# Kernel tuning notes

Hardware: AMD Instinct MI355X
Metric: run time of the kernel (lower is better)

## Reference

```python
import jax, jax.numpy as jnp
import numpy as np

HEADS = 8
NUM_CLASS = 4
DIM = 512


def setup_inputs() -> dict:
    key = jax.random.key(0)
    k0, k1, k2, k3 = jax.random.split(key, 4)
    B, N, C = 4, 1280, DIM  # N = (NUM_CLASS+1) * 256 tokens per group
    x = jax.random.normal(k0, (B, N, C), jnp.float32)
    # modality-presence mask: 1 = modality available, 0 = missing
    mask = jax.random.randint(k1, (B, NUM_CLASS), 0, 2).astype(jnp.int32)
    s = 1.0 / np.sqrt(C)
    W_qkv = jax.random.normal(k2, (C, 3 * C), jnp.float32) * s  # qkv (no bias)
    W_proj = jax.random.normal(k3, (C, C), jnp.float32) * s
    b_proj = jnp.zeros((C,), jnp.float32)
    return {"x": x, "mask": mask, "W_qkv": W_qkv, "W_proj": W_proj, "b_proj": b_proj}


def reference(x, mask, W_qkv, W_proj, b_proj):
    B, N, C = x.shape
    H = HEADS
    hd = C // H
    scale = hd ** -0.5
    # qkv: [B,N,3C] -> [3,B,H,N,hd]
    qkv = (x @ W_qkv).reshape(B, N, 3, H, hd).transpose(2, 0, 3, 1, 4)
    q, k, v = qkv[0], qkv[1], qkv[2]
    attn = jnp.einsum('bhqd,bhkd->bhqk', q, k) * scale  # [B,H,N,N]
    # block mask: keys belonging to missing modality groups are disallowed;
    # the last (fusion) group is always allowed -> every row has valid keys.
    np_ = N // (NUM_CLASS + 1)  # tokens per group
    group = jnp.arange(N) // np_  # [N], group id in [0, NUM_CLASS]
    allowed = jnp.concatenate(
        [mask.astype(jnp.float32), jnp.ones((B, 1), jnp.float32)], axis=1)  # [B, NUM_CLASS+1]
    col_ok = allowed[:, group]  # [B, N] per-key allowance
    attn = jnp.where(col_ok[:, None, None, :] == 0, -jnp.inf, attn)
    attn = jax.nn.softmax(attn, axis=-1)
    out = jnp.einsum('bhqk,bhkd->bhqd', attn, v)  # [B,H,N,hd]
    out = out.transpose(0, 2, 1, 3).reshape(B, N, C)
    out = out @ W_proj + b_proj
    return out, attn
```

## Files before the change

### kernel.cpp

```cpp
#include <hip/hip_runtime.h>
#include <math.h>

#define BATCH 4
#define NSEQ  1280
#define CDIM  512
#define HEADS 8
#define HD    64
#define NT    20
#define NQT   20

typedef __attribute__((ext_vector_type(8))) short bf16x8;
typedef __attribute__((ext_vector_type(4))) float f32x4;

#define MFMA16(a,b,c) __builtin_amdgcn_mfma_f32_16x16x32_bf16(a,b,c,0,0,0)

__device__ __forceinline__ unsigned short f2bf(float f) {
    union { float f; unsigned int u; } v; v.f = f;
    unsigned int r = v.u + 0x7fffu + ((v.u >> 16) & 1u);
    return (unsigned short)(r >> 16);
}
__device__ __forceinline__ float bf2f(unsigned short h) {
    union { unsigned int u; float f; } v; v.u = ((unsigned int)h) << 16;
    return v.f;
}
__device__ __forceinline__ void gload_lds16(const void* g, void* l) {
    __builtin_amdgcn_global_load_lds(
        (const __attribute__((address_space(1))) unsigned int*)g,
        (__attribute__((address_space(3))) unsigned int*)l, 16, 0, 0);
}

__global__ __launch_bounds__(256)
void conv_kernel(const float* __restrict__ x, const float* __restrict__ Wq,
                 const float* __restrict__ Wp, unsigned short* __restrict__ xb,
                 unsigned short* __restrict__ Wqt, unsigned short* __restrict__ Wpt)
{
    __shared__ float lt[64][65];
    const int bx = blockIdx.x;
    const int tid = threadIdx.x;
    if (bx < 1280) {
        const int u = bx * 256 + tid;
        const int m = u >> 6;
        const int b6 = u & 63;
        const int chunk = b6 >> 3;
        const int blk = b6 & 7;
        const float* src = x + (size_t)m * 512 + b6 * 8;
        bf16x8 hv;
        #pragma unroll
        for (int j = 0; j < 8; ++j) hv[j] = (short)f2bf(src[j]);
        *(bf16x8*)(xb + (size_t)m * 512 + chunk * 64 + ((blk ^ (m & 7)) * 8)) = hv;
    } else {
        int wi = bx - 1280;
        const float* W; unsigned short* Wt; int N, kt, nt; bool isQ;
        if (wi < 192) { W = Wq; Wt = Wqt; N = 1536; kt = wi / 24; nt = wi % 24; isQ = true; }
        else { wi -= 192; W = Wp; Wt = Wpt; N = 512; kt = wi / 8; nt = wi % 8; isQ = false; }
        const int k0 = kt * 64, n0 = nt * 64;
        {
            const int r = tid >> 4;
            const int c = (tid & 15) * 4;
            #pragma unroll
            for (int i = 0; i < 4; ++i) {
                const float4 v = *(const float4*)(W + (size_t)(k0 + r + i * 16) * N + n0 + c);
                lt[r + i * 16][c + 0] = v.x; lt[r + i * 16][c + 1] = v.y;
                lt[r + i * 16][c + 2] = v.z; lt[r + i * 16][c + 3] = v.w;
            }
        }
        __syncthreads();
        #pragma unroll
        for (int i = 0; i < 2; ++i) {
            const int u = tid + i * 256;
            const int n = u >> 3;
            const int blk = u & 7;
            const int kin = (blk ^ (n & 7)) * 8;
            const float sc = (isQ && (n0 + n) < 512) ? 0.125f : 1.0f;
            bf16x8 o;
            #pragma unroll
            for (int j = 0; j < 8; ++j) o[j] = (short)f2bf(lt[kin + j][n] * sc);
            *(bf16x8*)(Wt + (size_t)(n0 + n) * 512 + k0 + blk * 8) = o;
        }
    }
}

template<int WM, int WN, bool BIAS, bool OUTBF16>
__global__ __launch_bounds__(256)
void gemm_bf16(const unsigned short* __restrict__ A,
               const unsigned short* __restrict__ B,
               const float* __restrict__ bias, void* __restrict__ Cv,
               int M, int N, int KA)
{
    constexpr int BM = 2 * WM, BN = 2 * WN;
    constexpr int MI = WM / 16, NI = WN / 16;
    __shared__ __align__(16) unsigned short smem[(BM + BN) * 64];
    unsigned short* As = smem;
    unsigned short* Bs = smem + BM * 64;

    const int tid = threadIdx.x;
    const int w = tid >> 6, lane = tid & 63;
    const int l15 = lane & 15, hi = lane >> 4;
    const int wr = w >> 1, wc = w & 1;
    const int m0 = blockIdx.y * BM, n0 = blockIdx.x * BN;

    f32x4 acc[MI][NI];
    #pragma unroll
    for (int mi = 0; mi < MI; ++mi)
        #pragma unroll
        for (int ni = 0; ni < NI; ++ni) acc[mi][ni] = (f32x4){0.f, 0.f, 0.f, 0.f};

    constexpr int LA = BM * 128 / 4096;
    constexpr int LB = BN * 128 / 4096;

    for (int k0 = 0; k0 < KA; k0 += 64) {
        #pragma unroll
        for (int i = 0; i < LA; ++i) {
            const int off = tid * 16 + i * 4096;
            const int row = off >> 7, cb = off & 127;
            gload_lds16((const char*)A + ((size_t)(m0 + row) * KA + k0) * 2 + cb,
                        (char*)As + off);
        }
        #pragma unroll
        for (int i = 0; i < LB; ++i) {
            const int off = tid * 16 + i * 4096;
            const int row = off >> 7, cb = off & 127;
            gload_lds16((const char*)B + ((size_t)(n0 + row) * 512 + k0) * 2 + cb,
                        (char*)Bs + off);
        }
        __syncthreads();
        #pragma unroll
        for (int kk = 0; kk < 2; ++kk) {
            bf16x8 af[MI], bfr[NI];
            #pragma unroll
            for (int mi = 0; mi < MI; ++mi) {
                const int row = wr * WM + mi * 16 + l15;
                af[mi] = *(const bf16x8*)(As + row * 64 + ((kk * 4 + hi) ^ (row & 7)) * 8);
            }
            #pragma unroll
            for (int ni = 0; ni < NI; ++ni) {
                const int row = wc * WN + ni * 16 + l15;
                bfr[ni] = *(const bf16x8*)(Bs + row * 64 + ((kk * 4 + hi) ^ (row & 7)) * 8);
            }
            #pragma unroll
            for (int mi = 0; mi < MI; ++mi)
                #pragma unroll
                for (int ni = 0; ni < NI; ++ni)
                    acc[mi][ni] = MFMA16(af[mi], bfr[ni], acc[mi][ni]);
        }
        __syncthreads();
    }

    if (OUTBF16) {
        unsigned short* C = (unsigned short*)Cv;
        #pragma unroll
        for (int mi = 0; mi < MI; ++mi)
            #pragma unroll
            for (int ni = 0; ni < NI; ++ni)
                #pragma unroll
                for (int r = 0; r < 4; ++r)
                    smem[(wr * WM + mi * 16 + hi * 4 + r) * BN + wc * WN + ni * 16 + l15] =
                        f2bf(acc[mi][ni][r]);
        __syncthreads();
        constexpr int UNITS = BM * BN / 8 / 256;
        #pragma unroll
        for (int i = 0; i < UNITS; ++i) {
            const int u = tid + i * 256;
            const int row = u / (BN / 8), cb = u % (BN / 8);
            *(bf16x8*)(C + (size_t)(m0 + row) * N + n0 + cb * 8) =
                *(const bf16x8*)(smem + row * BN + cb * 8);
        }
    } else {
        float* C = (float*)Cv;
        #pragma unroll
        for (int mi = 0; mi < MI; ++mi)
            #pragma unroll
            for (int ni = 0; ni < NI; ++ni) {
                const int col = n0 + wc * WN + ni * 16 + l15;
                const float bv = BIAS ? bias[col] : 0.f;
                #pragma unroll
                for (int r = 0; r < 4; ++r)
                    C[(size_t)(m0 + wr * WM + mi * 16 + hi * 4 + r) * N + col] =
                        acc[mi][ni][r] + bv;
            }
    }
}

__global__ __launch_bounds__(256)
void vprep_kernel(const unsigned short* __restrict__ qkvb,
                  unsigned short* __restrict__ Vt)
{
    __shared__ __align__(16) unsigned short vt[64][72];
    const int bx = blockIdx.x;
    const int ntile = bx % NQT;
    const int bh = bx / NQT;
    const int b = bh >> 3, h = bh & 7;
    const int n0 = ntile * 64;
    const int tid = threadIdx.x;
    const unsigned short* base = qkvb + (size_t)(b * NSEQ + n0) * 1536 + 1024 + h * HD;

    #pragma unroll
    for (int i = 0; i < 2; ++i) {
        const int u = tid + i * 256;
        const int n = u >> 3;
        const int dg = u & 7;
        *(bf16x8*)&vt[n][dg * 8] = *(const bf16x8*)(base + (size_t)n * 1536 + dg * 8);
    }
    __syncthreads();
    #pragma unroll
    for (int i = 0; i < 2; ++i) {
        const int u = tid + i * 256;
        const int d = u >> 3;
        const int kb = u & 7;
        const int kin = (kb ^ (d & 7)) * 8;
        bf16x8 o;
        #pragma unroll
        for (int j = 0; j < 8; ++j) o[j] = (short)vt[kin + j][d];
        *(bf16x8*)(Vt + ((size_t)(bh * HD + d)) * NSEQ + n0 + kb * 8) = o;
    }
}

__global__ __launch_bounds__(256)
void attn_mfma(const unsigned short* __restrict__ qkvb,
               const unsigned short* __restrict__ Vt,
               const int* __restrict__ mask,
               float* __restrict__ attn, unsigned short* __restrict__ outh)
{
    __shared__ __align__(16) unsigned short kbuf[2][4096];
    __shared__ __align__(16) unsigned short vbuf[2][4096];
    __shared__ float ps[64][68];

    const int bx = blockIdx.x;
    const int qt = bx % NQT;
    const int bh = bx / NQT;
    const int b = bh >> 3, h = bh & 7;
    const int tid = threadIdx.x;
    const int w = tid >> 6;
    const int lane = tid & 63;
    const int l15 = lane & 15;
    const int hi = lane >> 4;
    const int q0 = qt * 64;

    unsigned int amask = 0xF0000u;
    #pragma unroll
    for (int g = 0; g < 4; ++g)
        if (mask[b * 4 + g] != 0) amask |= (0xFu << (g * 4));

    const unsigned short* qrow =
        qkvb + (size_t)(b * NSEQ + q0 + w * 16 + l15) * 1536 + h * HD;
    const bf16x8 aq0 = *(const bf16x8*)(qrow + hi * 8);
    const bf16x8 aq1 = *(const bf16x8*)(qrow + 32 + hi * 8);

    const unsigned short* ks = qkvb + (size_t)b * NSEQ * 1536 + 512 + h * HD;
    const unsigned short* vg = Vt + (size_t)bh * HD * NSEQ;

    #define STAGE_K(t, buf)                                                      \
        { _Pragma("unroll")                                                      \
          for (int half_ = 0; half_ < 2; ++half_) {                              \
            const int idx_ = half_ * 256 + tid;                                  \
            const int row_ = idx_ >> 3, blk_ = idx_ & 7;                         \
            gload_lds16(ks + (size_t)((t) * 64 + row_) * 1536                    \
                           + ((blk_ ^ (row_ & 7)) * 8),                          \
                        (char*)&(buf)[0] + idx_ * 16); } }
    #define STAGE_V(t, buf)                                                      \
        { _Pragma("unroll")                                                      \
          for (int half_ = 0; half_ < 2; ++half_) {                              \
            const int idx_ = half_ * 256 + tid;                                  \
            const int row_ = idx_ >> 3, blk_ = idx_ & 7;                         \
            gload_lds16(vg + (size_t)row_ * NSEQ + (t) * 64 + blk_ * 8,          \
                        (char*)&(buf)[0] + idx_ * 16); } }

    float lr[4] = {0.f, 0.f, 0.f, 0.f};

    int t0 = 0;
    while (!((amask >> t0) & 1u)) ++t0;

    STAGE_K(t0, kbuf[0]);
    __syncthreads();
    int cur = 0, t = t0;
    while (t < NT) {
        int tn = t + 1;
        while (tn < NT && !((amask >> tn) & 1u)) ++tn;
        if (tn < NT) STAGE_K(tn, kbuf[cur ^ 1]);
        f32x4 accS[4];
        #pragma unroll
        for (int cb = 0; cb < 4; ++cb) accS[cb] = (f32x4){0.f, 0.f, 0.f, 0.f};
        #pragma unroll
        for (int cb = 0; cb < 4; ++cb) {
            const int row = cb * 16 + l15;
            const char* bp = (const char*)&kbuf[cur][0] + row * 128;
            const bf16x8 b0 = *(const bf16x8*)(bp + ((hi ^ (row & 7)) * 16));
            const bf16x8 b1 = *(const bf16x8*)(bp + (((4 + hi) ^ (row & 7)) * 16));
            accS[cb] = MFMA16(aq0, b0, accS[cb]);
            accS[cb] = MFMA16(aq1, b1, accS[cb]);
        }
        #pragma unroll
        for (int cb = 0; cb < 4; ++cb)
            #pragma unroll
            for (int r = 0; r < 4; ++r)
                lr[r] += __expf(accS[cb][r]);
        __syncthreads();
        cur ^= 1; t = tn;
    }

    float rl[4];
    #pragma unroll
    for (int r = 0; r < 4; ++r) {
        float s = lr[r];
        s += __shfl_xor(s, 1);
        s += __shfl_xor(s, 2);
        s += __shfl_xor(s, 4);
        s += __shfl_xor(s, 8);
        rl[r] = 1.f / s;
    }

    {
        float* arow = attn + ((size_t)bh * NSEQ + q0 + w * 16) * NSEQ;
        const float4 z = make_float4(0.f, 0.f, 0.f, 0.f);
        for (int tz = 0; tz < NT; ++tz) {
            if ((amask >> tz) & 1u) continue;
            #pragma unroll
            for (int rr = 0; rr < 4; ++rr)
                *(float4*)(arow + (size_t)(rr * 4 + hi) * NSEQ + tz * 64 + l15 * 4) = z;
        }
    }

    STAGE_K(t0, kbuf[0]);
    STAGE_V(t0, vbuf[0]);
    __syncthreads();
    f32x4 accO[4];
    #pragma unroll
    for (int db = 0; db < 4; ++db) accO[db] = (f32x4){0.f, 0.f, 0.f, 0.f};

    cur = 0; t = t0;
    while (t < NT) {
        int tn = t + 1;
        while (tn < NT && !((amask >> tn) & 1u)) ++tn;
        if (tn < NT) {
            STAGE_K(tn, kbuf[cur ^ 1]);
            STAGE_V(tn, vbuf[cur ^ 1]);
        }
        f32x4 accS[4];
        #pragma unroll
        for (int cb = 0; cb < 4; ++cb) accS[cb] = (f32x4){0.f, 0.f, 0.f, 0.f};
        #pragma unroll
        for (int cb = 0; cb < 4; ++cb) {
            const int row = cb * 16 + l15;
            const char* bp = (const char*)&kbuf[cur][0] + row * 128;
            const bf16x8 b0 = *(const bf16x8*)(bp + ((hi ^ (row & 7)) * 16));
            const bf16x8 b1 = *(const bf16x8*)(bp + (((4 + hi) ^ (row & 7)) * 16));
            accS[cb] = MFMA16(aq0, b0, accS[cb]);
            accS[cb] = MFMA16(aq1, b1, accS[cb]);
        }
        #pragma unroll
        for (int cb = 0; cb < 4; ++cb)
            #pragma unroll
            for (int r = 0; r < 4; ++r)
                ps[w * 16 + hi * 4 + r][cb * 16 + l15] =
                    __expf(accS[cb][r]) * rl[r];

        {
            float* arow = attn + ((size_t)bh * NSEQ + q0 + w * 16) * NSEQ + t * 64;
            #pragma unroll
            for (int rr = 0; rr < 4; ++rr) {
                const float4 pv = *(const float4*)&ps[w * 16 + rr * 4 + hi][l15 * 4];
                *(float4*)(arow + (size_t)(rr * 4 + hi) * NSEQ + l15 * 4) = pv;
            }
        }

        #pragma unroll
        for (int s = 0; s < 2; ++s) {
            const float4 p0 = *(const float4*)&ps[w * 16 + l15][s * 32 + hi * 8];
            const float4 p1 = *(const float4*)&ps[w * 16 + l15][s * 32 + hi * 8 + 4];
            bf16x8 pa;
            pa[0] = (short)f2bf(p0.x); pa[1] = (short)f2bf(p0.y);
            pa[2] = (short)f2bf(p0.z); pa[3] = (short)f2bf(p0.w);
            pa[4] = (short)f2bf(p1.x); pa[5] = (short)f2bf(p1.y);
            pa[6] = (short)f2bf(p1.z); pa[7] = (short)f2bf(p1.w);
            #pragma unroll
            for (int db = 0; db < 4; ++db) {
                const int row = db * 16 + l15;
                const char* bp = (const char*)&vbuf[cur][0] + row * 128;
                const bf16x8 bv = *(const bf16x8*)(bp + (((4 * s + hi) ^ (row & 7)) * 16));
                accO[db] = MFMA16(pa, bv, accO[db]);
            }
        }
        __syncthreads();
        cur ^= 1; t = tn;
    }

    #pragma unroll
    for (int db = 0; db < 4; ++db)
        #pragma unroll
        for (int r = 0; r < 4; ++r)
            ps[w * 16 + hi * 4 + r][db * 16 + l15] = accO[db][r];
    #pragma unroll
    for (int i = 0; i < 2; ++i) {
        const int u = lane + i * 64;
        const int rowL = u >> 3;
        const int blk = u & 7;
        const float4 p0 = *(const float4*)&ps[w * 16 + rowL][blk * 8];
        const float4 p1 = *(const float4*)&ps[w * 16 + rowL][blk * 8 + 4];
        bf16x8 o;
        o[0] = (short)f2bf(p0.x); o[1] = (short)f2bf(p0.y);
        o[2] = (short)f2bf(p0.z); o[3] = (short)f2bf(p0.w);
        o[4] = (short)f2bf(p1.x); o[5] = (short)f2bf(p1.y);
        o[6] = (short)f2bf(p1.z); o[7] = (short)f2bf(p1.w);
        const int n = q0 + w * 16 + rowL;
        *(bf16x8*)(outh + ((size_t)(b * NSEQ + n)) * 512 + h * 64 + ((blk ^ (n & 7)) * 8)) = o;
    }
    #undef STAGE_K
    #undef STAGE_V
}

extern "C" void kernel_launch(void* const* d_in, const int* in_sizes, int n_in,
                              void* d_out, int out_size, void* d_ws, size_t ws_size,
                              hipStream_t stream)
{
    const float* x      = (const float*)d_in[0];
    const int*   mask   = (const int*)  d_in[1];
    const float* W_qkv  = (const float*)d_in[2];
    const float* W_proj = (const float*)d_in[3];
    const float* b_proj = (const float*)d_in[4];

    float* out  = (float*)d_out;
    float* attn = out + (size_t)BATCH * NSEQ * CDIM;

    char* ws = (char*)d_ws;
    unsigned short* qkvb = (unsigned short*)ws;
    unsigned short* Vt   = (unsigned short*)(ws + 15728640);
    unsigned short* xb   = (unsigned short*)(ws + 15728640 + 5242880);
    unsigned short* Wqt  = xb + (size_t)5120 * 512;
    unsigned short* Wpt  = Wqt + (size_t)1536 * 512;
    unsigned short* outh = Wpt + (size_t)512 * 512;

    const int M = BATCH * NSEQ;

    conv_kernel<<<1536, 256, 0, stream>>>(x, W_qkv, W_proj, xb, Wqt, Wpt);

    gemm_bf16<64, 64, false, true><<<dim3(1536 / 128, M / 128), 256, 0, stream>>>(
        xb, Wqt, nullptr, qkvb, M, 1536, 512);

    vprep_kernel<<<BATCH * HEADS * NQT, 256, 0, stream>>>(qkvb, Vt);

    attn_mfma<<<BATCH * HEADS * NQT, 256, 0, stream>>>(qkvb, Vt, mask, attn, outh);

    gemm_bf16<32, 64, true, false><<<dim3(512 / 128, M / 64), 256, 0, stream>>>(
        outh, Wpt, b_proj, out, M, 512, 512);
}
```

Before: 95.74 us.

## Enlarge attention and GEMM tiles, restructure MFMA loop and staged epilogue

The attention kernel now uses 512-thread blocks covering 128 query rows, so each staged K/V tile is shared by twice as many queries and fewer blocks are launched. The QKV GEMM widens its N tile and the projection GEMM doubles its M tile, and the GEMM inner loop loads one B fragment at a time to reduce register pressure. The bf16 epilogue writes through shared memory one 16-row slab per step, so the smem buffer fits the larger tile. The larger blocks may lower occupancy or leave fewer blocks than there are CUs.

```diff
diff --git a/kernel.cpp b/kernel.cpp
--- a/kernel.cpp
+++ b/kernel.cpp
@@ -8,6 +8,7 @@
 #define HD    64
 #define NT    20
 #define NQT   20
+#define NQTA  10
 
 typedef __attribute__((ext_vector_type(8))) short bf16x8;
 typedef __attribute__((ext_vector_type(4))) float f32x4;
@@ -126,7 +127,7 @@
         __syncthreads();
         #pragma unroll
         for (int kk = 0; kk < 2; ++kk) {
-            bf16x8 af[MI], bfr[NI];
+            bf16x8 af[MI];
             #pragma unroll
             for (int mi = 0; mi < MI; ++mi) {
                 const int row = wr * WM + mi * 16 + l15;
@@ -135,13 +136,12 @@
             #pragma unroll
             for (int ni = 0; ni < NI; ++ni) {
                 const int row = wc * WN + ni * 16 + l15;
-                bfr[ni] = *(const bf16x8*)(Bs + row * 64 + ((kk * 4 + hi) ^ (row & 7)) * 8);
-            }
-            #pragma unroll
-            for (int mi = 0; mi < MI; ++mi)
+                const bf16x8 bfr =
+                    *(const bf16x8*)(Bs + row * 64 + ((kk * 4 + hi) ^ (row & 7)) * 8);
                 #pragma unroll
-                for (int ni = 0; ni < NI; ++ni)
-                    acc[mi][ni] = MFMA16(af[mi], bfr[ni], acc[mi][ni]);
+                for (int mi = 0; mi < MI; ++mi)
+                    acc[mi][ni] = MFMA16(af[mi], bfr, acc[mi][ni]);
+            }
         }
         __syncthreads();
     }
@@ -149,21 +149,24 @@
     if (OUTBF16) {
         unsigned short* C = (unsigned short*)Cv;
         #pragma unroll
-        for (int mi = 0; mi < MI; ++mi)
+        for (int mi = 0; mi < MI; ++mi) {
+            __syncthreads();
             #pragma unroll
             for (int ni = 0; ni < NI; ++ni)
                 #pragma unroll
                 for (int r = 0; r < 4; ++r)
-                    smem[(wr * WM + mi * 16 + hi * 4 + r) * BN + wc * WN + ni * 16 + l15] =
+                    smem[(wr * 16 + hi * 4 + r) * BN + wc * WN + ni * 16 + l15] =
                         f2bf(acc[mi][ni][r]);
-        __syncthreads();
-        constexpr int UNITS = BM * BN / 8 / 256;
-        #pragma unroll
-        for (int i = 0; i < UNITS; ++i) {
-            const int u = tid + i * 256;
-            const int row = u / (BN / 8), cb = u % (BN / 8);
-            *(bf16x8*)(C + (size_t)(m0 + row) * N + n0 + cb * 8) =
-                *(const bf16x8*)(smem + row * BN + cb * 8);
+            __syncthreads();
+            constexpr int UNITS = 32 * (BN / 8) / 256;
+            #pragma unroll
+            for (int i = 0; i < UNITS; ++i) {
+                const int u = tid + i * 256;
+                const int srow = u / (BN / 8), cb = u % (BN / 8);
+                const int grow = m0 + (srow >> 4) * WM + mi * 16 + (srow & 15);
+                *(bf16x8*)(C + (size_t)grow * N + n0 + cb * 8) =
+                    *(const bf16x8*)(smem + srow * BN + cb * 8);
+            }
         }
     } else {
         float* C = (float*)Cv;
@@ -215,7 +218,7 @@
     }
 }
 
-__global__ __launch_bounds__(256)
+__global__ __launch_bounds__(512)
 void attn_mfma(const unsigned short* __restrict__ qkvb,
                const unsigned short* __restrict__ Vt,
                const int* __restrict__ mask,
@@ -223,18 +226,18 @@
 {
     __shared__ __align__(16) unsigned short kbuf[2][4096];
     __shared__ __align__(16) unsigned short vbuf[2][4096];
-    __shared__ float ps[64][68];
+    __shared__ float ps[128][68];
 
     const int bx = blockIdx.x;
-    const int qt = bx % NQT;
-    const int bh = bx / NQT;
+    const int qt = bx % NQTA;
+    const int bh = bx / NQTA;
     const int b = bh >> 3, h = bh & 7;
     const int tid = threadIdx.x;
     const int w = tid >> 6;
     const int lane = tid & 63;
     const int l15 = lane & 15;
     const int hi = lane >> 4;
-    const int q0 = qt * 64;
+    const int q0 = qt * 128;
 
     unsigned int amask = 0xF0000u;
     #pragma unroll
@@ -250,20 +253,14 @@
     const unsigned short* vg = Vt + (size_t)bh * HD * NSEQ;
 
     #define STAGE_K(t, buf)                                                      \
-        { _Pragma("unroll")                                                      \
-          for (int half_ = 0; half_ < 2; ++half_) {                              \
-            const int idx_ = half_ * 256 + tid;                                  \
-            const int row_ = idx_ >> 3, blk_ = idx_ & 7;                         \
-            gload_lds16(ks + (size_t)((t) * 64 + row_) * 1536                    \
-                           + ((blk_ ^ (row_ & 7)) * 8),                          \
-                        (char*)&(buf)[0] + idx_ * 16); } }
+        { const int row_ = tid >> 3, blk_ = tid & 7;                             \
+          gload_lds16(ks + (size_t)((t) * 64 + row_) * 1536                      \
+                         + ((blk_ ^ (row_ & 7)) * 8),                            \
+                      (char*)&(buf)[0] + tid * 16); }
     #define STAGE_V(t, buf)                                                      \
-        { _Pragma("unroll")                                                      \
-          for (int half_ = 0; half_ < 2; ++half_) {                              \
-            const int idx_ = half_ * 256 + tid;                                  \
-            const int row_ = idx_ >> 3, blk_ = idx_ & 7;                         \
-            gload_lds16(vg + (size_t)row_ * NSEQ + (t) * 64 + blk_ * 8,          \
-                        (char*)&(buf)[0] + idx_ * 16); } }
+        { const int row_ = tid >> 3, blk_ = tid & 7;                             \
+          gload_lds16(vg + (size_t)row_ * NSEQ + (t) * 64 + blk_ * 8,            \
+                      (char*)&(buf)[0] + tid * 16); }
 
     float lr[4] = {0.f, 0.f, 0.f, 0.f};
 
@@ -433,13 +430,13 @@
 
     conv_kernel<<<1536, 256, 0, stream>>>(x, W_qkv, W_proj, xb, Wqt, Wpt);
 
-    gemm_bf16<64, 64, false, true><<<dim3(1536 / 128, M / 128), 256, 0, stream>>>(
+    gemm_bf16<64, 128, false, true><<<dim3(1536 / 256, M / 128), 256, 0, stream>>>(
         xb, Wqt, nullptr, qkvb, M, 1536, 512);
 
     vprep_kernel<<<BATCH * HEADS * NQT, 256, 0, stream>>>(qkvb, Vt);
 
-    attn_mfma<<<BATCH * HEADS * NQT, 256, 0, stream>>>(qkvb, Vt, mask, attn, outh);
-
-    gemm_bf16<32, 64, true, false><<<dim3(512 / 128, M / 64), 256, 0, stream>>>(
+    attn_mfma<<<BATCH * HEADS * NQTA, 512, 0, stream>>>(qkvb, Vt, mask, attn, outh);
+
+    gemm_bf16<64, 64, true, false><<<dim3(512 / 128, M / 128), 256, 0, stream>>>(
         outh, Wpt, b_proj, out, M, 512, 512);
 }
```

After: 110.0 us. 1.15x slower.
